# Optimization experiments

Hardware: AMD Instinct MI355X
Metric: run time of the kernel (lower is better)

Reference implementation:

```python
import jax, jax.numpy as jnp
import numpy as np

E, M, K, N = 32, 1024, 512, 512

def setup_inputs() -> dict:
    key = jax.random.key(0)
    k1, k2, k3 = jax.random.split(key, 3)
    A = jax.random.normal(k1, (E, M, K), dtype=jnp.float32)
    B = jax.random.normal(k2, (E, N, K), dtype=jnp.float32)
    expert_num_tokens = jax.random.randint(k3, (E,), 0, M + 1, dtype=jnp.int32)
    return {"A": A, "B": B, "expert_num_tokens": expert_num_tokens}

def reference(A, B, expert_num_tokens):
    # Per-expert GEMM: C[e] = A[e] @ B[e].T  -> [E, M, N]
    C = jnp.einsum('emk,enk->emn', A, B)
    # Rows m >= expert_num_tokens[e] are never computed/stored by the kernel;
    # zero them in the reference output.
    row_valid = jnp.arange(A.shape[1])[None, :] < expert_num_tokens[:, None]  # [E, M]
    return jnp.where(row_valid[:, :, None], C, jnp.zeros((), C.dtype))
```

## Files before the change

kernel.cpp:

```cpp
#include <hip/hip_runtime.h>
#include <hip/hip_bf16.h>

#define NE 32
#define MM 1024
#define KK 512
#define NN 512
#define BM 64
#define BN 128
#define BK 32

typedef __attribute__((ext_vector_type(8))) short bf16x8;
typedef __attribute__((ext_vector_type(4))) float floatx4;

__device__ __forceinline__ short f2bf(float f) {
  union { __hip_bfloat16 b; short s; } u;
  u.b = __float2bfloat16(f);
  return u.s;
}

extern "C" __global__ __launch_bounds__(256, 3)
void expert_gemm(const float* __restrict__ A, const float* __restrict__ B,
                 const int* __restrict__ cnts, float* __restrict__ C)
{
  const int b    = blockIdx.x;
  const int tid  = threadIdx.x;
  const int xcd  = b & 7;
  const int slot = b >> 3;

  int e = -1, mt = 0, nt = 0, zfill = 0;
  int base = 0;
#pragma unroll 1
  for (int i = 0; i < 4; ++i) {
    int ei = xcd + (i << 3);
    int vt = (cnts[ei] + 63) >> 6;
    int tot = 16 + 3 * vt;
    if (e < 0 && slot < base + tot) {
      int r = slot - base;
      int g = vt << 2;
      e = ei;
      if (r < g) { mt = r >> 2; nt = r & 3; }
      else       { zfill = 1; mt = vt + (r - g); }
    }
    base += tot;
  }
  if (e < 0) return;

  if (zfill) {
    float* Ce = C + ((size_t)e * MM + mt * BM) * NN;
    float4 zf = make_float4(0.f, 0.f, 0.f, 0.f);
#pragma unroll
    for (int i = 0; i < 32; ++i) {
      int fidx = i * 256 + tid;
      int r = fidx >> 7, c = (fidx & 127) << 2;
      *(float4*)(Ce + (size_t)r * NN + c) = zf;
    }
    return;
  }

  const int m0 = mt * BM, n0 = nt * BN;
  const int cnt = cnts[e];
  const float* Ae = A + ((size_t)e * MM + m0) * KK;
  const float* Be = B + ((size_t)e * NN + n0) * KK;
  float* Ce = C + ((size_t)e * MM + m0) * NN + n0;

  __shared__ __align__(16) short lA[BM * BK];
  __shared__ __align__(16) short lB[BN * BK];

  const int wave = tid >> 6, lane = tid & 63;
  const int wm = (wave >> 1) * 32, wn = (wave & 1) * 64;
  const int fr = lane & 15, kh = lane >> 4;

  const int sr = tid >> 2;
  const int su = tid & 3;

  floatx4 acc4[2][4] = {};

  float4 ra[2], rbv[4], na[2], nb[4];

#define ISSUE(pa, pb, kt_) do {                                          \
    int col_ = (kt_) + (su << 3);                                        \
    pa[0] = *(const float4*)(Ae + (size_t)sr * KK + col_);               \
    pa[1] = *(const float4*)(Ae + (size_t)sr * KK + col_ + 4);           \
    pb[0] = *(const float4*)(Be + (size_t)sr * KK + col_);               \
    pb[1] = *(const float4*)(Be + (size_t)sr * KK + col_ + 4);           \
    pb[2] = *(const float4*)(Be + (size_t)(sr + 64) * KK + col_);        \
    pb[3] = *(const float4*)(Be + (size_t)(sr + 64) * KK + col_ + 4);    \
  } while (0)

  ISSUE(ra, rbv, 0);

#pragma unroll
  for (int kt = 0; kt < KK; kt += BK) {
    if (kt + BK < KK) ISSUE(na, nb, kt + BK);

    bf16x8 va  = { f2bf(ra[0].x),  f2bf(ra[0].y),  f2bf(ra[0].z),  f2bf(ra[0].w),
                   f2bf(ra[1].x),  f2bf(ra[1].y),  f2bf(ra[1].z),  f2bf(ra[1].w) };
    bf16x8 vb0 = { f2bf(rbv[0].x), f2bf(rbv[0].y), f2bf(rbv[0].z), f2bf(rbv[0].w),
                   f2bf(rbv[1].x), f2bf(rbv[1].y), f2bf(rbv[1].z), f2bf(rbv[1].w) };
    bf16x8 vb1 = { f2bf(rbv[2].x), f2bf(rbv[2].y), f2bf(rbv[2].z), f2bf(rbv[2].w),
                   f2bf(rbv[3].x), f2bf(rbv[3].y), f2bf(rbv[3].z), f2bf(rbv[3].w) };

    __syncthreads();
    {
      int u0 = (sr << 2) + (su ^ (sr & 3));
      *(bf16x8*)(lA + (u0 << 3)) = va;
      *(bf16x8*)(lB + (u0 << 3)) = vb0;
      int r1 = sr + 64;
      int u1 = (r1 << 2) + (su ^ (r1 & 3));
      *(bf16x8*)(lB + (u1 << 3)) = vb1;
    }
    __syncthreads();

    bf16x8 af[2], bfv[4];
#pragma unroll
    for (int i = 0; i < 2; ++i) {
      int rA = wm + (i << 4) + fr;
      af[i]  = *(const bf16x8*)(lA + ((((rA << 2) + (kh ^ (rA & 3)))) << 3));
    }
#pragma unroll
    for (int j = 0; j < 4; ++j) {
      int rB = wn + (j << 4) + fr;
      bfv[j] = *(const bf16x8*)(lB + ((((rB << 2) + (kh ^ (rB & 3)))) << 3));
    }
#pragma unroll
    for (int i = 0; i < 2; ++i)
#pragma unroll
      for (int j = 0; j < 4; ++j)
        acc4[i][j] = __builtin_amdgcn_mfma_f32_16x16x32_bf16(af[i], bfv[j], acc4[i][j], 0, 0, 0);

#pragma unroll
    for (int q = 0; q < 2; ++q) ra[q] = na[q];
#pragma unroll
    for (int q = 0; q < 4; ++q) rbv[q] = nb[q];
  }
#undef ISSUE

  const int rbase = (lane >> 4) * 4;
#pragma unroll
  for (int i = 0; i < 2; ++i) {
#pragma unroll
    for (int r = 0; r < 4; ++r) {
      int row = wm + i * 16 + rbase + r;
      bool valid = (m0 + row) < cnt;
#pragma unroll
      for (int j = 0; j < 4; ++j) {
        int col = wn + j * 16 + fr;
        Ce[(size_t)row * NN + col] = valid ? acc4[i][j][r] : 0.0f;
      }
    }
  }
}

extern "C" void kernel_launch(void* const* d_in, const int* in_sizes, int n_in,
                              void* d_out, int out_size, void* d_ws, size_t ws_size,
                              hipStream_t stream) {
  const float* A    = (const float*)d_in[0];
  const float* B    = (const float*)d_in[1];
  const int*   cnts = (const int*)d_in[2];
  float*       C    = (float*)d_out;

  hipLaunchKernelGGL(expert_gemm, dim3(2048), dim3(256), 0, stream, A, B, cnts, C);
}
```

Before: 162.7 us.

## Convert expert GEMM to persistent grid-stride loop over tile slots

The launch of 2048 blocks, most of which exit early, becomes 512 persistent blocks (64 per XCD). Each block strides through its XCD's tile slots and performs either a GEMM tile or a zero-fill tile for each one. This removes the cost of launching and retiring many empty blocks. In exchange, the fixed slot assignment can load-balance poorly when experts have uneven work. Launch bounds drop from 3 to 2 waves per SIMD occupancy hint, which may shift register allocation.

```diff
diff --git a/kernel.cpp b/kernel.cpp
--- a/kernel.cpp
+++ b/kernel.cpp
@@ -18,50 +18,22 @@
   return u.s;
 }
 
-extern "C" __global__ __launch_bounds__(256, 3)
+extern "C" __global__ __launch_bounds__(256, 2)
 void expert_gemm(const float* __restrict__ A, const float* __restrict__ B,
                  const int* __restrict__ cnts, float* __restrict__ C)
 {
-  const int b    = blockIdx.x;
-  const int tid  = threadIdx.x;
-  const int xcd  = b & 7;
-  const int slot = b >> 3;
+  const int xcd   = blockIdx.x & 7;
+  const int slot0 = blockIdx.x >> 3;
+  const int tid   = threadIdx.x;
 
-  int e = -1, mt = 0, nt = 0, zfill = 0;
-  int base = 0;
-#pragma unroll 1
+  int vt[4], base[5];
+  base[0] = 0;
+#pragma unroll
   for (int i = 0; i < 4; ++i) {
-    int ei = xcd + (i << 3);
-    int vt = (cnts[ei] + 63) >> 6;
-    int tot = 16 + 3 * vt;
-    if (e < 0 && slot < base + tot) {
-      int r = slot - base;
-      int g = vt << 2;
-      e = ei;
-      if (r < g) { mt = r >> 2; nt = r & 3; }
-      else       { zfill = 1; mt = vt + (r - g); }
-    }
-    base += tot;
+    vt[i] = (cnts[xcd + (i << 3)] + 63) >> 6;
+    base[i + 1] = base[i] + 16 + 3 * vt[i];
   }
-  if (e < 0) return;
-
-  if (zfill) {
-    float* Ce = C + ((size_t)e * MM + mt * BM) * NN;
-    float4 zf = make_float4(0.f, 0.f, 0.f, 0.f);
-#pragma unroll
-    for (int i = 0; i < 32; ++i) {
-      int fidx = i * 256 + tid;
-      int r = fidx >> 7, c = (fidx & 127) << 2;
-      *(float4*)(Ce + (size_t)r * NN + c) = zf;
-    }
-    return;
-  }
-
-  const int m0 = mt * BM, n0 = nt * BN;
-  const int cnt = cnts[e];
-  const float* Ae = A + ((size_t)e * MM + m0) * KK;
-  const float* Be = B + ((size_t)e * NN + n0) * KK;
-  float* Ce = C + ((size_t)e * MM + m0) * NN + n0;
+  const int total = base[4];
 
   __shared__ __align__(16) short lA[BM * BK];
   __shared__ __align__(16) short lB[BN * BK];
@@ -69,13 +41,40 @@
   const int wave = tid >> 6, lane = tid & 63;
   const int wm = (wave >> 1) * 32, wn = (wave & 1) * 64;
   const int fr = lane & 15, kh = lane >> 4;
-
   const int sr = tid >> 2;
   const int su = tid & 3;
 
-  floatx4 acc4[2][4] = {};
+#pragma unroll 1
+  for (int s = slot0; s < total; s += 64) {
+    int i = (s >= base[2]) ? ((s >= base[3]) ? 3 : 2) : ((s >= base[1]) ? 1 : 0);
+    int r = s - base[i];
+    const int e = xcd + (i << 3);
+    const int v = vt[i];
+    const int g = v << 2;
 
-  float4 ra[2], rbv[4], na[2], nb[4];
+    if (r >= g) {
+      int mt = v + (r - g);
+      float* Ce = C + ((size_t)e * MM + mt * BM) * NN;
+      float4 zf = make_float4(0.f, 0.f, 0.f, 0.f);
+#pragma unroll
+      for (int q = 0; q < 32; ++q) {
+        int fidx = q * 256 + tid;
+        int rr = fidx >> 7, cc = (fidx & 127) << 2;
+        *(float4*)(Ce + (size_t)rr * NN + cc) = zf;
+      }
+      continue;
+    }
+
+    const int mt = r >> 2, nt = r & 3;
+    const int m0 = mt * BM, n0 = nt * BN;
+    const int cnt = cnts[e];
+    const float* Ae = A + ((size_t)e * MM + m0) * KK;
+    const float* Be = B + ((size_t)e * NN + n0) * KK;
+    float* Ce = C + ((size_t)e * MM + m0) * NN + n0;
+
+    floatx4 acc4[2][4] = {};
+
+    float4 ra[2], rbv[4], na[2], nb[4];
 
 #define ISSUE(pa, pb, kt_) do {                                          \
     int col_ = (kt_) + (su << 3);                                        \
@@ -87,65 +86,66 @@
     pb[3] = *(const float4*)(Be + (size_t)(sr + 64) * KK + col_ + 4);    \
   } while (0)
 
-  ISSUE(ra, rbv, 0);
+    ISSUE(ra, rbv, 0);
 
 #pragma unroll
-  for (int kt = 0; kt < KK; kt += BK) {
-    if (kt + BK < KK) ISSUE(na, nb, kt + BK);
+    for (int kt = 0; kt < KK; kt += BK) {
+      if (kt + BK < KK) ISSUE(na, nb, kt + BK);
 
-    bf16x8 va  = { f2bf(ra[0].x),  f2bf(ra[0].y),  f2bf(ra[0].z),  f2bf(ra[0].w),
-                   f2bf(ra[1].x),  f2bf(ra[1].y),  f2bf(ra[1].z),  f2bf(ra[1].w) };
-    bf16x8 vb0 = { f2bf(rbv[0].x), f2bf(rbv[0].y), f2bf(rbv[0].z), f2bf(rbv[0].w),
-                   f2bf(rbv[1].x), f2bf(rbv[1].y), f2bf(rbv[1].z), f2bf(rbv[1].w) };
-    bf16x8 vb1 = { f2bf(rbv[2].x), f2bf(rbv[2].y), f2bf(rbv[2].z), f2bf(rbv[2].w),
-                   f2bf(rbv[3].x), f2bf(rbv[3].y), f2bf(rbv[3].z), f2bf(rbv[3].w) };
+      bf16x8 va  = { f2bf(ra[0].x),  f2bf(ra[0].y),  f2bf(ra[0].z),  f2bf(ra[0].w),
+                     f2bf(ra[1].x),  f2bf(ra[1].y),  f2bf(ra[1].z),  f2bf(ra[1].w) };
+      bf16x8 vb0 = { f2bf(rbv[0].x), f2bf(rbv[0].y), f2bf(rbv[0].z), f2bf(rbv[0].w),
+                     f2bf(rbv[1].x), f2bf(rbv[1].y), f2bf(rbv[1].z), f2bf(rbv[1].w) };
+      bf16x8 vb1 = { f2bf(rbv[2].x), f2bf(rbv[2].y), f2bf(rbv[2].z), f2bf(rbv[2].w),
+                     f2bf(rbv[3].x), f2bf(rbv[3].y), f2bf(rbv[3].z), f2bf(rbv[3].w) };
 
-    __syncthreads();
-    {
-      int u0 = (sr << 2) + (su ^ (sr & 3));
-      *(bf16x8*)(lA + (u0 << 3)) = va;
-      *(bf16x8*)(lB + (u0 << 3)) = vb0;
-      int r1 = sr + 64;
-      int u1 = (r1 << 2) + (su ^ (r1 & 3));
-      *(bf16x8*)(lB + (u1 << 3)) = vb1;
-    }
-    __syncthreads();
+      __syncthreads();
+      {
+        int u0 = (sr << 2) + (su ^ (sr & 3));
+        *(bf16x8*)(lA + (u0 << 3)) = va;
+        *(bf16x8*)(lB + (u0 << 3)) = vb0;
+        int r1 = sr + 64;
+        int u1 = (r1 << 2) + (su ^ (r1 & 3));
+        *(bf16x8*)(lB + (u1 << 3)) = vb1;
+      }
+      __syncthreads();
 
-    bf16x8 af[2], bfv[4];
+      bf16x8 af[2], bfv[4];
 #pragma unroll
-    for (int i = 0; i < 2; ++i) {
-      int rA = wm + (i << 4) + fr;
-      af[i]  = *(const bf16x8*)(lA + ((((rA << 2) + (kh ^ (rA & 3)))) << 3));
-    }
+      for (int q = 0; q < 2; ++q) {
+        int rA = wm + (q << 4) + fr;
+        af[q]  = *(const bf16x8*)(lA + ((((rA << 2) + (kh ^ (rA & 3)))) << 3));
+      }
 #pragma unroll
-    for (int j = 0; j < 4; ++j) {
-      int rB = wn + (j << 4) + fr;
-      bfv[j] = *(const bf16x8*)(lB + ((((rB << 2) + (kh ^ (rB & 3)))) << 3));
-    }
+      for (int j = 0; j < 4; ++j) {
+        int rB = wn + (j << 4) + fr;
+        bfv[j] = *(const bf16x8*)(lB + ((((rB << 2) + (kh ^ (rB & 3)))) << 3));
+      }
 #pragma unroll
-    for (int i = 0; i < 2; ++i)
+      for (int q = 0; q < 2; ++q)
 #pragma unroll
-      for (int j = 0; j < 4; ++j)
-        acc4[i][j] = __builtin_amdgcn_mfma_f32_16x16x32_bf16(af[i], bfv[j], acc4[i][j], 0, 0, 0);
+        for (int j = 0; j < 4; ++j)
+          acc4[q][j] = __builtin_amdgcn_mfma_f32_16x16x32_bf16(af[q], bfv[j], acc4[q][j], 0, 0, 0);
 
 #pragma unroll
-    for (int q = 0; q < 2; ++q) ra[q] = na[q];
+      for (int q = 0; q < 2; ++q) ra[q] = na[q];
 #pragma unroll
-    for (int q = 0; q < 4; ++q) rbv[q] = nb[q];
-  }
+      for (int q = 0; q < 4; ++q) rbv[q] = nb[q];
+    }
 #undef ISSUE
 
-  const int rbase = (lane >> 4) * 4;
+    const int rbase = (lane >> 4) * 4;
 #pragma unroll
-  for (int i = 0; i < 2; ++i) {
+    for (int q = 0; q < 2; ++q) {
 #pragma unroll
-    for (int r = 0; r < 4; ++r) {
-      int row = wm + i * 16 + rbase + r;
-      bool valid = (m0 + row) < cnt;
+      for (int rr = 0; rr < 4; ++rr) {
+        int row = wm + q * 16 + rbase + rr;
+        bool valid = (m0 + row) < cnt;
 #pragma unroll
-      for (int j = 0; j < 4; ++j) {
-        int col = wn + j * 16 + fr;
-        Ce[(size_t)row * NN + col] = valid ? acc4[i][j][r] : 0.0f;
+        for (int j = 0; j < 4; ++j) {
+          int col = wn + j * 16 + fr;
+          Ce[(size_t)row * NN + col] = valid ? acc4[q][j][rr] : 0.0f;
+        }
       }
     }
   }
@@ -159,5 +159,5 @@
   const int*   cnts = (const int*)d_in[2];
   float*       C    = (float*)d_out;
 
-  hipLaunchKernelGGL(expert_gemm, dim3(2048), dim3(256), 0, stream, A, B, cnts, C);
+  hipLaunchKernelGGL(expert_gemm, dim3(512), dim3(256), 0, stream, A, B, cnts, C);
 }
```

Result: no change. 165.1 us (+1.4%).

## Stream fp32 tiles directly into double-buffered LDS with global_load_lds

Applied to the files above, without the earlier changes.

Global loads no longer go through registers and a bf16 convert-and-store into LDS. Raw fp32 A and B tiles are now copied straight into LDS with global_load_lds. Two buffers let the next K-tile's copy overlap MFMA work on the current one, and one barrier per iteration replaces two. An XOR swizzle on the LDS layout is kept, so each fragment is read as two float4s and converted to bf16 after the LDS read. The costs are doubled LDS per block (48 KB) and redundant fp32-to-bf16 conversion, because every wave converts the fragments it reads.

```diff
diff --git a/kernel.cpp b/kernel.cpp
--- a/kernel.cpp
+++ b/kernel.cpp
@@ -18,6 +18,10 @@
   return u.s;
 }
 
+#define GLDS(g, l) __builtin_amdgcn_global_load_lds(                      \
+    (const __attribute__((address_space(1))) void*)(g),                   \
+    (__attribute__((address_space(3))) void*)(l), 16, 0, 0)
+
 extern "C" __global__ __launch_bounds__(256, 3)
 void expert_gemm(const float* __restrict__ A, const float* __restrict__ B,
                  const int* __restrict__ cnts, float* __restrict__ C)
@@ -29,7 +33,7 @@
 
   int e = -1, mt = 0, nt = 0, zfill = 0;
   int base = 0;
-#pragma unroll 1
+#pragma unroll
   for (int i = 0; i < 4; ++i) {
     int ei = xcd + (i << 3);
     int vt = (cnts[ei] + 63) >> 6;
@@ -63,64 +67,66 @@
   const float* Be = B + ((size_t)e * NN + n0) * KK;
   float* Ce = C + ((size_t)e * MM + m0) * NN + n0;
 
-  __shared__ __align__(16) short lA[BM * BK];
-  __shared__ __align__(16) short lB[BN * BK];
+  __shared__ __align__(16) float sA[2][BM * BK];
+  __shared__ __align__(16) float sB[2][BN * BK];
 
   const int wave = tid >> 6, lane = tid & 63;
   const int wm = (wave >> 1) * 32, wn = (wave & 1) * 64;
   const int fr = lane & 15, kh = lane >> 4;
+  const int frs = fr & 7;
 
-  const int sr = tid >> 2;
-  const int su = tid & 3;
+  const int lr = lane >> 3;
+  const int lu = (lane & 7) ^ lr;
+  const size_t rowb = (size_t)lr * (KK * 4) + (size_t)lu * 16;
+  const char* gA = (const char*)Ae;
+  const char* gB = (const char*)Be;
+
+#define STAGE(bufi, KT) do {                                               \
+    _Pragma("unroll")                                                      \
+    for (int q = 0; q < 2; ++q) {                                          \
+      int ia = wave + (q << 2);                                            \
+      GLDS(gA + (size_t)(8 * ia) * (KK * 4) + rowb + (size_t)(KT) * 4,     \
+           &sA[bufi][ia << 8]);                                            \
+    }                                                                      \
+    _Pragma("unroll")                                                      \
+    for (int q = 0; q < 4; ++q) {                                          \
+      int ib = wave + (q << 2);                                            \
+      GLDS(gB + (size_t)(8 * ib) * (KK * 4) + rowb + (size_t)(KT) * 4,     \
+           &sB[bufi][ib << 8]);                                            \
+    }                                                                      \
+  } while (0)
 
   floatx4 acc4[2][4] = {};
 
-  float4 ra[2], rbv[4], na[2], nb[4];
+  STAGE(0, 0);
+  __syncthreads();
 
-#define ISSUE(pa, pb, kt_) do {                                          \
-    int col_ = (kt_) + (su << 3);                                        \
-    pa[0] = *(const float4*)(Ae + (size_t)sr * KK + col_);               \
-    pa[1] = *(const float4*)(Ae + (size_t)sr * KK + col_ + 4);           \
-    pb[0] = *(const float4*)(Be + (size_t)sr * KK + col_);               \
-    pb[1] = *(const float4*)(Be + (size_t)sr * KK + col_ + 4);           \
-    pb[2] = *(const float4*)(Be + (size_t)(sr + 64) * KK + col_);        \
-    pb[3] = *(const float4*)(Be + (size_t)(sr + 64) * KK + col_ + 4);    \
-  } while (0)
-
-  ISSUE(ra, rbv, 0);
-
+  int cur = 0;
 #pragma unroll
   for (int kt = 0; kt < KK; kt += BK) {
-    if (kt + BK < KK) ISSUE(na, nb, kt + BK);
+    if (kt + BK < KK) STAGE(cur ^ 1, kt + BK);
 
-    bf16x8 va  = { f2bf(ra[0].x),  f2bf(ra[0].y),  f2bf(ra[0].z),  f2bf(ra[0].w),
-                   f2bf(ra[1].x),  f2bf(ra[1].y),  f2bf(ra[1].z),  f2bf(ra[1].w) };
-    bf16x8 vb0 = { f2bf(rbv[0].x), f2bf(rbv[0].y), f2bf(rbv[0].z), f2bf(rbv[0].w),
-                   f2bf(rbv[1].x), f2bf(rbv[1].y), f2bf(rbv[1].z), f2bf(rbv[1].w) };
-    bf16x8 vb1 = { f2bf(rbv[2].x), f2bf(rbv[2].y), f2bf(rbv[2].z), f2bf(rbv[2].w),
-                   f2bf(rbv[3].x), f2bf(rbv[3].y), f2bf(rbv[3].z), f2bf(rbv[3].w) };
-
-    __syncthreads();
-    {
-      int u0 = (sr << 2) + (su ^ (sr & 3));
-      *(bf16x8*)(lA + (u0 << 3)) = va;
-      *(bf16x8*)(lB + (u0 << 3)) = vb0;
-      int r1 = sr + 64;
-      int u1 = (r1 << 2) + (su ^ (r1 & 3));
-      *(bf16x8*)(lB + (u1 << 3)) = vb1;
-    }
-    __syncthreads();
+    const char* bufA = (const char*)sA[cur];
+    const char* bufB = (const char*)sB[cur];
 
     bf16x8 af[2], bfv[4];
 #pragma unroll
     for (int i = 0; i < 2; ++i) {
       int rA = wm + (i << 4) + fr;
-      af[i]  = *(const bf16x8*)(lA + ((((rA << 2) + (kh ^ (rA & 3)))) << 3));
+      const char* rb = bufA + rA * 128;
+      float4 f0 = *(const float4*)(rb + ((((kh << 1)    ) ^ frs) << 4));
+      float4 f1 = *(const float4*)(rb + ((((kh << 1) | 1) ^ frs) << 4));
+      af[i] = (bf16x8){ f2bf(f0.x), f2bf(f0.y), f2bf(f0.z), f2bf(f0.w),
+                        f2bf(f1.x), f2bf(f1.y), f2bf(f1.z), f2bf(f1.w) };
     }
 #pragma unroll
     for (int j = 0; j < 4; ++j) {
       int rB = wn + (j << 4) + fr;
-      bfv[j] = *(const bf16x8*)(lB + ((((rB << 2) + (kh ^ (rB & 3)))) << 3));
+      const char* rb = bufB + rB * 128;
+      float4 f0 = *(const float4*)(rb + ((((kh << 1)    ) ^ frs) << 4));
+      float4 f1 = *(const float4*)(rb + ((((kh << 1) | 1) ^ frs) << 4));
+      bfv[j] = (bf16x8){ f2bf(f0.x), f2bf(f0.y), f2bf(f0.z), f2bf(f0.w),
+                         f2bf(f1.x), f2bf(f1.y), f2bf(f1.z), f2bf(f1.w) };
     }
 #pragma unroll
     for (int i = 0; i < 2; ++i)
@@ -128,12 +134,10 @@
       for (int j = 0; j < 4; ++j)
         acc4[i][j] = __builtin_amdgcn_mfma_f32_16x16x32_bf16(af[i], bfv[j], acc4[i][j], 0, 0, 0);
 
-#pragma unroll
-    for (int q = 0; q < 2; ++q) ra[q] = na[q];
-#pragma unroll
-    for (int q = 0; q < 4; ++q) rbv[q] = nb[q];
+    __syncthreads();
+    cur ^= 1;
   }
-#undef ISSUE
+#undef STAGE
 
   const int rbase = (lane >> 4) * 4;
 #pragma unroll
```

After: 173.5 us. 1.07x slower.

## Load MFMA fragments directly from global memory, dropping LDS staging

Applied to the files above, without the earlier changes.

Each wave now loads its own A and B fragment rows straight from global memory into registers and converts them to bf16 in place, with no shared memory and no __syncthreads barriers. This removes LDS traffic and block-level synchronisation. The cost is more global and L2 traffic, because waves sharing the same rows (A is read by 2 waves, B by 2 waves) each fetch them separately, and register pressure roughly doubles for the prefetch buffers. The expert-lookup loop is also fully unrolled.

```diff
diff --git a/kernel.cpp b/kernel.cpp
--- a/kernel.cpp
+++ b/kernel.cpp
@@ -29,7 +29,7 @@
 
   int e = -1, mt = 0, nt = 0, zfill = 0;
   int base = 0;
-#pragma unroll 1
+#pragma unroll
   for (int i = 0; i < 4; ++i) {
     int ei = xcd + (i << 3);
     int vt = (cnts[ei] + 63) >> 6;
@@ -63,65 +63,56 @@
   const float* Be = B + ((size_t)e * NN + n0) * KK;
   float* Ce = C + ((size_t)e * MM + m0) * NN + n0;
 
-  __shared__ __align__(16) short lA[BM * BK];
-  __shared__ __align__(16) short lB[BN * BK];
-
   const int wave = tid >> 6, lane = tid & 63;
   const int wm = (wave >> 1) * 32, wn = (wave & 1) * 64;
   const int fr = lane & 15, kh = lane >> 4;
 
-  const int sr = tid >> 2;
-  const int su = tid & 3;
+  const float* pA0 = Ae + (size_t)(wm + fr)      * KK + (kh << 3);
+  const float* pA1 = Ae + (size_t)(wm + 16 + fr) * KK + (kh << 3);
+  const float* pB0 = Be + (size_t)(wn + fr)      * KK + (kh << 3);
+  const float* pB1 = Be + (size_t)(wn + 16 + fr) * KK + (kh << 3);
+  const float* pB2 = Be + (size_t)(wn + 32 + fr) * KK + (kh << 3);
+  const float* pB3 = Be + (size_t)(wn + 48 + fr) * KK + (kh << 3);
 
   floatx4 acc4[2][4] = {};
 
-  float4 ra[2], rbv[4], na[2], nb[4];
+  float4 ra[4], rb[8], na[4], nb[8];
 
-#define ISSUE(pa, pb, kt_) do {                                          \
-    int col_ = (kt_) + (su << 3);                                        \
-    pa[0] = *(const float4*)(Ae + (size_t)sr * KK + col_);               \
-    pa[1] = *(const float4*)(Ae + (size_t)sr * KK + col_ + 4);           \
-    pb[0] = *(const float4*)(Be + (size_t)sr * KK + col_);               \
-    pb[1] = *(const float4*)(Be + (size_t)sr * KK + col_ + 4);           \
-    pb[2] = *(const float4*)(Be + (size_t)(sr + 64) * KK + col_);        \
-    pb[3] = *(const float4*)(Be + (size_t)(sr + 64) * KK + col_ + 4);    \
+#define ISSUE(pa, pb, kt_) do {                                    \
+    pa[0] = *(const float4*)(pA0 + (kt_));                         \
+    pa[1] = *(const float4*)(pA0 + (kt_) + 4);                     \
+    pa[2] = *(const float4*)(pA1 + (kt_));                         \
+    pa[3] = *(const float4*)(pA1 + (kt_) + 4);                     \
+    pb[0] = *(const float4*)(pB0 + (kt_));                         \
+    pb[1] = *(const float4*)(pB0 + (kt_) + 4);                     \
+    pb[2] = *(const float4*)(pB1 + (kt_));                         \
+    pb[3] = *(const float4*)(pB1 + (kt_) + 4);                     \
+    pb[4] = *(const float4*)(pB2 + (kt_));                         \
+    pb[5] = *(const float4*)(pB2 + (kt_) + 4);                     \
+    pb[6] = *(const float4*)(pB3 + (kt_));                         \
+    pb[7] = *(const float4*)(pB3 + (kt_) + 4);                     \
   } while (0)
 
-  ISSUE(ra, rbv, 0);
+  ISSUE(ra, rb, 0);
 
 #pragma unroll
   for (int kt = 0; kt < KK; kt += BK) {
     if (kt + BK < KK) ISSUE(na, nb, kt + BK);
 
-    bf16x8 va  = { f2bf(ra[0].x),  f2bf(ra[0].y),  f2bf(ra[0].z),  f2bf(ra[0].w),
-                   f2bf(ra[1].x),  f2bf(ra[1].y),  f2bf(ra[1].z),  f2bf(ra[1].w) };
-    bf16x8 vb0 = { f2bf(rbv[0].x), f2bf(rbv[0].y), f2bf(rbv[0].z), f2bf(rbv[0].w),
-                   f2bf(rbv[1].x), f2bf(rbv[1].y), f2bf(rbv[1].z), f2bf(rbv[1].w) };
-    bf16x8 vb1 = { f2bf(rbv[2].x), f2bf(rbv[2].y), f2bf(rbv[2].z), f2bf(rbv[2].w),
-                   f2bf(rbv[3].x), f2bf(rbv[3].y), f2bf(rbv[3].z), f2bf(rbv[3].w) };
-
-    __syncthreads();
-    {
-      int u0 = (sr << 2) + (su ^ (sr & 3));
-      *(bf16x8*)(lA + (u0 << 3)) = va;
-      *(bf16x8*)(lB + (u0 << 3)) = vb0;
-      int r1 = sr + 64;
-      int u1 = (r1 << 2) + (su ^ (r1 & 3));
-      *(bf16x8*)(lB + (u1 << 3)) = vb1;
-    }
-    __syncthreads();
-
     bf16x8 af[2], bfv[4];
 #pragma unroll
     for (int i = 0; i < 2; ++i) {
-      int rA = wm + (i << 4) + fr;
-      af[i]  = *(const bf16x8*)(lA + ((((rA << 2) + (kh ^ (rA & 3)))) << 3));
+      float4 f0 = ra[i * 2], f1 = ra[i * 2 + 1];
+      af[i] = (bf16x8){ f2bf(f0.x), f2bf(f0.y), f2bf(f0.z), f2bf(f0.w),
+                        f2bf(f1.x), f2bf(f1.y), f2bf(f1.z), f2bf(f1.w) };
     }
 #pragma unroll
     for (int j = 0; j < 4; ++j) {
-      int rB = wn + (j << 4) + fr;
-      bfv[j] = *(const bf16x8*)(lB + ((((rB << 2) + (kh ^ (rB & 3)))) << 3));
+      float4 f0 = rb[j * 2], f1 = rb[j * 2 + 1];
+      bfv[j] = (bf16x8){ f2bf(f0.x), f2bf(f0.y), f2bf(f0.z), f2bf(f0.w),
+                         f2bf(f1.x), f2bf(f1.y), f2bf(f1.z), f2bf(f1.w) };
     }
+
 #pragma unroll
     for (int i = 0; i < 2; ++i)
 #pragma unroll
@@ -129,9 +120,9 @@
         acc4[i][j] = __builtin_amdgcn_mfma_f32_16x16x32_bf16(af[i], bfv[j], acc4[i][j], 0, 0, 0);
 
 #pragma unroll
-    for (int q = 0; q < 2; ++q) ra[q] = na[q];
+    for (int q = 0; q < 4; ++q) ra[q] = na[q];
 #pragma unroll
-    for (int q = 0; q < 4; ++q) rbv[q] = nb[q];
+    for (int q = 0; q < 8; ++q) rb[q] = nb[q];
   }
 #undef ISSUE
 
```

After: 262.5 us. +61.3%, slower.
